# Kernel tuning notes

Hardware: AMD Instinct MI355X
Metric: run time of the kernel (lower is better)

## Reference

```python
import jax, jax.numpy as jnp
from jax import lax
import numpy as np

B, N, E, U = 128, 1024, 300, 128
L = 512          # num_leaves per sample
NN = 2 * L - 1   # num_nodes per sample (binary tree)


def _hsig(x):
    # Keras hard_sigmoid: clip(0.2*x + 0.5, 0, 1)
    return jnp.clip(0.2 * x + 0.5, 0.0, 1.0)


def setup_inputs() -> dict:
    key = jax.random.key(0)
    ks = jax.random.split(key, 5)
    rng = np.random.default_rng(0)
    # children of node t are uniform in [0, t) -> valid bottom-up binary tree
    u = rng.random((B, N, 2))
    child = (u * np.arange(N)[None, :, None]).astype(np.int32)
    child[:, :L, :] = 0  # leaves have no children (never read)
    num_vecs = np.tile(np.array([[NN, L]], np.int32), (B, 1))
    return {
        "initial_state": jax.random.normal(ks[0], (B, N, E), jnp.float32),
        "translation_kernel": jax.random.normal(ks[1], (E, U), jnp.float32) * 0.05,
        "kernel": jax.random.normal(ks[2], (5 * U, U), jnp.float32) * 0.05,
        "recurrent_kernel": jax.random.normal(ks[3], (5 * U, 2 * U), jnp.float32) * 0.05,
        "bias": jnp.zeros((5 * U, 1), jnp.float32),
        "child_vecs": jnp.asarray(child),
        "num_vecs": jnp.asarray(num_vecs),
    }


def reference(initial_state, translation_kernel, kernel, recurrent_kernel, bias,
              child_vecs, num_vecs):
    b, n, _ = initial_state.shape
    units = kernel.shape[1]
    # leaf initial states: relu(x @ W_translate)  -> [B, N, U]
    x = jax.nn.relu(jnp.einsum('bne,eu->bnu', initial_state, translation_kernel))
    num_nodes = num_vecs[:, 0]
    num_leaves = num_vecs[:, 1]
    bvec = bias[:, 0][None, :]  # [1, 5U]

    def step(carry, t):
        H, C = carry  # [B, N, U] each
        ch = jnp.take(child_vecs, t, axis=1)                                   # [B, 2]
        h_ch = jnp.take_along_axis(H, ch[:, :, None], axis=1).reshape(b, 2 * units)
        c_ch = jnp.take_along_axis(C, ch[:, :, None], axis=1).reshape(b, 2 * units)
        xt = jnp.take(x, t, axis=1)                                            # [B, U]
        # z = kernel @ x^T + recurrent_kernel @ [h_l; h_r] + bias  (batched, [B, 5U])
        z = xt @ kernel.T + h_ch @ recurrent_kernel.T + bvec
        i = _hsig(z[:, :units])
        f = _hsig(z[:, units:3 * units])                                       # [B, 2U]
        o = _hsig(z[:, 3 * units:4 * units])
        g = jnp.tanh(z[:, 4 * units:])
        # faithful to original: reshape (flat_mem*f) as [U, 2] row-major, sum axis 1
        c_new = (c_ch * f).reshape(b, units, 2).sum(axis=-1) + i * g
        h_new = o * jnp.tanh(c_new)
        act = ((t >= num_leaves) & (t < num_nodes))[:, None]                   # [B, 1]
        h_upd = jnp.where(act, h_new, jnp.take(H, t, axis=1))
        c_upd = jnp.where(act, c_new, jnp.take(C, t, axis=1))
        H = lax.dynamic_update_slice(H, h_upd[:, None, :], (0, t, 0))
        C = lax.dynamic_update_slice(C, c_upd[:, None, :], (0, t, 0))
        return (H, C), None

    # leaves start with hidden = memory = translated vec; internal nodes overwritten in order
    (H, _), _ = lax.scan(step, (x, x), jnp.arange(n))
    valid = (jnp.arange(n)[None, :] < num_nodes[:, None])[..., None]
    return H * valid.astype(H.dtype)
```

## Files before the change

### kernel.cpp

```cpp
#include <hip/hip_runtime.h>
#include <hip/hip_bf16.h>

#define B_ 128
#define N_ 1024
#define E_ 300
#define U_ 128
#define M_ (B_ * N_)
#define Z_ (5 * U_)
#define LMAXT 40
#define LPAR 14

typedef __attribute__((ext_vector_type(8))) short bf16x8;
typedef __attribute__((ext_vector_type(4))) float f32x4;
typedef _Float16 h2_t __attribute__((ext_vector_type(2)));
typedef _Float16 f16x4 __attribute__((ext_vector_type(4)));
typedef _Float16 f16x8 __attribute__((ext_vector_type(8)));

__device__ __forceinline__ short f2bf(float f) {
  unsigned u = __builtin_bit_cast(unsigned, f);
  u = (u + 0x7fffu + ((u >> 16) & 1u)) >> 16;
  return (short)u;
}

__device__ __forceinline__ float hsig(float z) {
  float v = __builtin_fmaf(z, 0.2f, 0.5f);
  v = v < 0.f ? 0.f : v;
  v = v > 1.f ? 1.f : v;
  return v;
}

__device__ __forceinline__ float tanh_fast(float x) {
  float p = __expf(2.f * x);
  return 1.f - 2.f * __builtin_amdgcn_rcpf(p + 1.f);
}

__device__ __forceinline__ unsigned pk2(float a, float b) {
  return __builtin_bit_cast(unsigned, __builtin_amdgcn_cvt_pkrtz(a, b));
}

__global__ __launch_bounds__(256) void x_gemm(
    const float* __restrict__ A, const float* __restrict__ W,
    float* __restrict__ H, float* __restrict__ C) {
  __shared__ __align__(16) short As[64][40];
  __shared__ __align__(16) short Ws[128][40];
  const int tid = threadIdx.x;
  const int m0 = blockIdx.x * 64;
  f32x4 acc[8] = {};
  const int lane = tid & 63, wv = tid >> 6;
  const int lr = lane & 15, lg = lane >> 4;

  for (int kc = 0; kc < 10; ++kc) {
    const int k0 = kc * 32;
    {
      const int row = tid >> 2, kk = (tid & 3) * 8;
      const float* src = A + (size_t)(m0 + row) * E_ + k0 + kk;
      bf16x8 v;
      if (k0 + 32 <= E_) {
#pragma unroll
        for (int i = 0; i < 8; ++i) v[i] = f2bf(src[i]);
      } else {
#pragma unroll
        for (int i = 0; i < 8; ++i)
          v[i] = (k0 + kk + i < E_) ? f2bf(src[i]) : (short)0;
      }
      *(bf16x8*)&As[row][kk] = v;
    }
#pragma unroll
    for (int s = 0; s < 2; ++s) {
      const int slot = tid + s * 256;
      const int n = slot & 127, kg = slot >> 7;
      bf16x8 v;
      if (k0 + 32 <= E_) {
#pragma unroll
        for (int i = 0; i < 8; ++i) v[i] = f2bf(W[(k0 + kg * 8 + i) * U_ + n]);
      } else {
#pragma unroll
        for (int i = 0; i < 8; ++i) {
          const int k = k0 + kg * 8 + i;
          v[i] = (k < E_) ? f2bf(W[k * U_ + n]) : (short)0;
        }
      }
      *(bf16x8*)&Ws[n][kg * 8] = v;
    }
    __syncthreads();
    bf16x8 a = *(const bf16x8*)&As[wv * 16 + lr][lg * 8];
#pragma unroll
    for (int nt = 0; nt < 8; ++nt) {
      bf16x8 b = *(const bf16x8*)&Ws[nt * 16 + lr][lg * 8];
      acc[nt] = __builtin_amdgcn_mfma_f32_16x16x32_bf16(a, b, acc[nt], 0, 0, 0);
    }
    __syncthreads();
  }
#pragma unroll
  for (int nt = 0; nt < 8; ++nt) {
#pragma unroll
    for (int r = 0; r < 4; ++r) {
      const int m = m0 + wv * 16 + lg * 4 + r;
      const int n = nt * 16 + lr;
      float v = acc[nt][r];
      v = v > 0.f ? v : 0.f;
      H[(size_t)m * U_ + n] = v;
      C[(size_t)m * U_ + n] = v;
    }
  }
}

__global__ __launch_bounds__(256) void xz_gemm(
    const float* __restrict__ X, const float* __restrict__ K,
    const float* __restrict__ bias, const int* __restrict__ nv,
    _Float16* __restrict__ XZ) {
  const int m0 = blockIdx.x * 64;
  {
    const int bb = m0 >> 10;
    const int t0 = m0 & (N_ - 1);
    const int nodes = nv[2 * bb], leaves = nv[2 * bb + 1];
    if (t0 + 64 <= leaves || t0 >= nodes) return;
  }
  __shared__ __align__(16) short As[64][40];
  __shared__ __align__(16) short Ws[128][40];
  const int tid = threadIdx.x;
  const int n0 = blockIdx.y * 128;
  f32x4 acc[8] = {};
  const int lane = tid & 63, wv = tid >> 6;
  const int lr = lane & 15, lg = lane >> 4;

  for (int kc = 0; kc < 4; ++kc) {
    const int k0 = kc * 32;
    {
      const int row = tid >> 2, kk = (tid & 3) * 8;
      const float* src = X + (size_t)(m0 + row) * U_ + k0 + kk;
      bf16x8 v;
#pragma unroll
      for (int i = 0; i < 8; ++i) v[i] = f2bf(src[i]);
      *(bf16x8*)&As[row][kk] = v;
    }
#pragma unroll
    for (int s = 0; s < 2; ++s) {
      const int slot = tid + s * 256;
      const int n = slot >> 2, kk = (slot & 3) * 8;
      const float* src = K + (size_t)(n0 + n) * U_ + k0 + kk;
      bf16x8 v;
#pragma unroll
      for (int i = 0; i < 8; ++i) v[i] = f2bf(src[i]);
      *(bf16x8*)&Ws[n][kk] = v;
    }
    __syncthreads();
    bf16x8 a = *(const bf16x8*)&As[wv * 16 + lr][lg * 8];
#pragma unroll
    for (int nt = 0; nt < 8; ++nt) {
      bf16x8 b = *(const bf16x8*)&Ws[nt * 16 + lr][lg * 8];
      acc[nt] = __builtin_amdgcn_mfma_f32_16x16x32_bf16(a, b, acc[nt], 0, 0, 0);
    }
    __syncthreads();
  }
#pragma unroll
  for (int nt = 0; nt < 8; ++nt) {
    const int n = n0 + nt * 16 + lr;
    const float bv = bias[n];
#pragma unroll
    for (int r = 0; r < 4; ++r) {
      const int m = m0 + wv * 16 + lg * 4 + r;
      XZ[(size_t)m * Z_ + n] = (_Float16)(acc[nt][r] + bv);
    }
  }
}

__global__ __launch_bounds__(256) void wcvt(const float* __restrict__ Wr,
                                            _Float16* __restrict__ W16) {
  const int i = (blockIdx.x * 256 + threadIdx.x) * 2;
  if (i < 640 * 256) {
    W16[i] = (_Float16)Wr[i];
    W16[i + 1] = (_Float16)Wr[i + 1];
  }
}

__global__ __launch_bounds__(512) void levelize(
    const int* __restrict__ child, const int* __restrict__ nv,
    int* __restrict__ lv, int* __restrict__ rank, int* __restrict__ cnt) {
  const int b = blockIdx.x;
  const int tid = threadIdx.x;
  int nodes = nv[2 * b];
  int leaves = nv[2 * b + 1];
  if (nodes > N_) nodes = N_;
  if (leaves < 0) leaves = 0;

  __shared__ short lvs[N_];
  __shared__ int chs[2 * N_];
  __shared__ int cnts[LMAXT];
  __shared__ int changed;

  for (int i = tid; i < N_; i += 512) lvs[i] = 0;
  for (int i = tid; i < 2 * N_; i += 512) chs[i] = child[(size_t)b * 2 * N_ + i];
  if (tid < LMAXT) cnts[tid] = 0;
  __syncthreads();

  int stable = 0;
  for (int s = 0; s < 64; ++s) {
    if (tid == 0) changed = 0;
    __syncthreads();
    int any = 0;
    for (int t = leaves + tid; t < nodes; t += 512) {
      const int c0 = chs[2 * t], c1 = chs[2 * t + 1];
      const int l0 = (c0 < t && c0 >= 0) ? lvs[c0] : 0;
      const int l1 = (c1 < t && c1 >= 0) ? lvs[c1] : 0;
      const int l = 1 + (l0 > l1 ? l0 : l1);
      if (l > (int)lvs[t]) { lvs[t] = (short)l; any = 1; }
    }
    if (any) changed = 1;
    __syncthreads();
    if (!changed) { stable = 1; break; }
  }
  if (!stable) {
    if (tid == 0) {
      for (int t = leaves; t < nodes; ++t) {
        const int c0 = chs[2 * t], c1 = chs[2 * t + 1];
        const int l0 = (c0 < t && c0 >= 0) ? lvs[c0] : 0;
        const int l1 = (c1 < t && c1 >= 0) ? lvs[c1] : 0;
        lvs[t] = (short)(1 + (l0 > l1 ? l0 : l1));
      }
    }
    __syncthreads();
  }

  for (int t = leaves + tid; t < nodes; t += 512) {
    int l = lvs[t];
    if (l > LMAXT - 1) l = LMAXT - 1;
    lv[b * N_ + t] = l;
    if (l < LMAXT - 1) rank[b * N_ + t] = atomicAdd(&cnts[l], 1);
  }
  __syncthreads();
  if (tid == 0) {
    for (int t = leaves; t < nodes; ++t)
      if ((int)lvs[t] >= LMAXT - 1) rank[b * N_ + t] = cnts[LMAXT - 1]++;
  }
  __syncthreads();
  if (tid < LMAXT) cnt[tid * 128 + b] = cnts[tid];
}

__global__ __launch_bounds__(64) void offsets(
    const int* __restrict__ cnt, int* __restrict__ pos, int* __restrict__ goff) {
  const int l = threadIdx.x;
  __shared__ int tot[LMAXT];
  if (l < LMAXT) {
    int s = 0;
    for (int b = 0; b < 128; ++b) {
      pos[l * 128 + b] = s;
      s += cnt[l * 128 + b];
    }
    tot[l] = s;
  }
  __syncthreads();
  if (l == 0) {
    int g = 0;
    for (int i = 0; i < LMAXT; ++i) { goff[i] = g; g += tot[i]; }
    goff[LMAXT] = g;
  }
  __syncthreads();
  if (l < LMAXT) {
    const int g = goff[l];
    for (int b = 0; b < 128; ++b) pos[l * 128 + b] += g;
  }
}

__global__ __launch_bounds__(256) void scatter_zero(
    const int* __restrict__ nv, const int* __restrict__ lv,
    const int* __restrict__ rank, const int* __restrict__ pos,
    int* __restrict__ glist, float* __restrict__ H) {
  const int b = blockIdx.x;
  const int tid = threadIdx.x;
  int nodes = nv[2 * b];
  int leaves = nv[2 * b + 1];
  if (nodes > N_) nodes = N_;
  if (leaves < 0) leaves = 0;
  for (int t = leaves + tid; t < nodes; t += 256) {
    const int l = lv[b * N_ + t];
    glist[pos[l * 128 + b] + rank[b * N_ + t]] = (b << 10) | t;
  }
  const int total = (N_ - nodes) * U_;
  for (int idx = tid; idx < total; idx += 256)
    H[(size_t)b * N_ * U_ + nodes * U_ + idx] = 0.f;
}

__global__ __launch_bounds__(512, 2) void level_gemm(
    int lvl, const _Float16* __restrict__ W16, const int* __restrict__ child,
    const int* __restrict__ goff, const int* __restrict__ glist,
    const _Float16* __restrict__ XZ, float* __restrict__ H,
    float* __restrict__ C) {
  const int base = goff[lvl];
  const int count = goff[lvl + 1] - base;
  if (count <= 0) return;
  const int tid = threadIdx.x;
  const int lane = tid & 63, w = tid >> 6;
  const int col = lane & 15, hi = lane >> 4;
  const int u0 = 16 * w + 4 * hi;
  const int mc = 2 * u0;

  f16x8 afrag[5][8];
  {
    const int rows[5] = {16 * w + col, 128 + 32 * w + 2 * col,
                         129 + 32 * w + 2 * col, 384 + 16 * w + col,
                         512 + 16 * w + col};
#pragma unroll
    for (int rt = 0; rt < 5; ++rt) {
      const _Float16* rs = W16 + (size_t)rows[rt] * 256 + 8 * hi;
#pragma unroll
      for (int kt = 0; kt < 8; ++kt) afrag[rt][kt] = *(const f16x8*)(rs + 32 * kt);
    }
  }

  __shared__ __align__(16) _Float16 hbuf[16][272];

  const int nchunk = (count + 15) >> 4;
  for (int chunk = blockIdx.x; chunk < nchunk; chunk += gridDim.x) {
    const int cb = base + chunk * 16;
    int rem = count - chunk * 16;
    if (rem > 16) rem = 16;

    const int j = tid >> 5, s = tid & 31;
    const int nidj = glist[cb + (j < rem ? j : rem - 1)];
    const int bj = nidj >> 10, tj = nidj & 1023;
    const int chj = child[((size_t)bj << 11) + 2 * tj + (s >> 4)];
    const float* hsrc =
        H + (((size_t)(bj << 10) + chj) << 7) + ((s & 15) << 3);
    const float4 a0 = *(const float4*)hsrc;
    const float4 a1 = *(const float4*)(hsrc + 4);

    const int nidc = glist[cb + (col < rem ? col : rem - 1)];
    const int bc = nidc >> 10, tc = nidc & 1023;
    const _Float16* xzr = XZ + ((size_t)((bc << 10) | tc)) * Z_;
    const f16x4 xzi = *(const f16x4*)(xzr + u0);
    const f16x8 xzf = *(const f16x8*)(xzr + 128 + mc);
    const f16x4 xzo = *(const f16x4*)(xzr + 384 + u0);
    const f16x4 xzg = *(const f16x4*)(xzr + 512 + u0);
    const int csel = child[((size_t)bc << 11) + 2 * tc + (mc >> 7)];
    const float* cbp = C + (((size_t)(bc << 10) + csel) << 7) + (mc & 127);
    const float4 cv0 = ((const float4*)cbp)[0];
    const float4 cv1 = ((const float4*)cbp)[1];

    uint4 hp;
    hp.x = pk2(a0.x, a0.y);
    hp.y = pk2(a0.z, a0.w);
    hp.z = pk2(a1.x, a1.y);
    hp.w = pk2(a1.z, a1.w);
    *(uint4*)&hbuf[j][(s >> 4) * 128 + (s & 15) * 8] = hp;
    __syncthreads();

    f32x4 acc[5];
#pragma unroll
    for (int r = 0; r < 4; ++r) {
      acc[0][r] = (float)xzi[r];
      acc[1][r] = (float)xzf[2 * r];
      acc[2][r] = (float)xzf[2 * r + 1];
      acc[3][r] = (float)xzo[r];
      acc[4][r] = (float)xzg[r];
    }
#pragma unroll
    for (int kt = 0; kt < 8; ++kt) {
      const f16x8 bf = *(const f16x8*)&hbuf[col][32 * kt + 8 * hi];
#pragma unroll
      for (int rt = 0; rt < 5; ++rt)
        acc[rt] = __builtin_amdgcn_mfma_f32_16x16x32_f16(afrag[rt][kt], bf,
                                                         acc[rt], 0, 0, 0);
    }

    const float ce[8] = {cv0.x, cv0.y, cv0.z, cv0.w,
                         cv1.x, cv1.y, cv1.z, cv1.w};
    f32x4 hn4, cn4;
#pragma unroll
    for (int r = 0; r < 4; ++r) {
      const float cn = ce[2 * r] * hsig(acc[1][r]) +
                       ce[2 * r + 1] * hsig(acc[2][r]) +
                       hsig(acc[0][r]) * tanh_fast(acc[4][r]);
      cn4[r] = cn;
      hn4[r] = hsig(acc[3][r]) * tanh_fast(cn);
    }
    if (col < rem) {
      const size_t rowb = ((size_t)((bc << 10) | tc)) << 7;
      *(f32x4*)(H + rowb + u0) = hn4;
      *(f32x4*)(C + rowb + u0) = cn4;
    }
    __syncthreads();
  }
}

__global__ __launch_bounds__(512, 2) void tail_scan(
    const _Float16* __restrict__ W16, const int* __restrict__ child,
    const int* __restrict__ nv, const int* __restrict__ pos,
    const int* __restrict__ cnt, const int* __restrict__ glist,
    const _Float16* __restrict__ XZ, float* __restrict__ H,
    float* __restrict__ C) {
  const int b = blockIdx.x;
  const int tid = threadIdx.x;
  const int lane = tid & 63, w = tid >> 6;
  const int col = lane & 15, hi = lane >> 4;
  const int u0 = 16 * w + 4 * hi;
  const int mc = 2 * u0;
  const int m4 = 4 * lane;

  f16x8 afrag[5][8];
  {
    const int rows[5] = {16 * w + col, 128 + 32 * w + 2 * col,
                         129 + 32 * w + 2 * col, 384 + 16 * w + col,
                         512 + 16 * w + col};
#pragma unroll
    for (int rt = 0; rt < 5; ++rt) {
      const _Float16* rs = W16 + (size_t)rows[rt] * 256 + 8 * hi;
#pragma unroll
      for (int kt = 0; kt < 8; ++kt) afrag[rt][kt] = *(const f16x8*)(rs + 32 * kt);
    }
  }

  __shared__ __align__(16) _Float16 hb1[256];
  const int* chb = child + (size_t)b * 2 * N_;
  float* Hb = H + (size_t)b * N_ * U_;
  float* Cb = C + (size_t)b * N_ * U_;
  const _Float16* xzb = XZ + (size_t)b * N_ * Z_;

  for (int l = LPAR; l < LMAXT; ++l) {
    const int p0 = pos[l * 128 + b];
    const int n = cnt[l * 128 + b];
    for (int i = 0; i < n; ++i) {
      const int t = glist[p0 + i] & 1023;
      if (tid < 64) {
        const int ch = chb[2 * t + (m4 >> 7)];
        const float4 hv = *(const float4*)(Hb + ((size_t)ch << 7) + (m4 & 127));
        uint2 hp;
        hp.x = pk2(hv.x, hv.y);
        hp.y = pk2(hv.z, hv.w);
        *(uint2*)&hb1[m4] = hp;
      }
      const int cs = chb[2 * t + (mc >> 7)];
      const float* cbp = Cb + ((size_t)cs << 7) + (mc & 127);
      const float4 cv0 = ((const float4*)cbp)[0];
      const float4 cv1 = ((const float4*)cbp)[1];
      const _Float16* xzr = xzb + (size_t)t * Z_;
      const f16x4 xzi = *(const f16x4*)(xzr + u0);
      const f16x8 xzf = *(const f16x8*)(xzr + 128 + mc);
      const f16x4 xzo = *(const f16x4*)(xzr + 384 + u0);
      const f16x4 xzg = *(const f16x4*)(xzr + 512 + u0);
      __syncthreads();
      f32x4 acc[5];
#pragma unroll
      for (int r = 0; r < 4; ++r) {
        acc[0][r] = (float)xzi[r];
        acc[1][r] = (float)xzf[2 * r];
        acc[2][r] = (float)xzf[2 * r + 1];
        acc[3][r] = (float)xzo[r];
        acc[4][r] = (float)xzg[r];
      }
#pragma unroll
      for (int kt = 0; kt < 8; ++kt) {
        const f16x8 bf = *(const f16x8*)&hb1[32 * kt + 8 * hi];
#pragma unroll
        for (int rt = 0; rt < 5; ++rt)
          acc[rt] = __builtin_amdgcn_mfma_f32_16x16x32_f16(afrag[rt][kt], bf,
                                                           acc[rt], 0, 0, 0);
      }
      const float ce[8] = {cv0.x, cv0.y, cv0.z, cv0.w,
                           cv1.x, cv1.y, cv1.z, cv1.w};
      f32x4 hn4, cn4;
#pragma unroll
      for (int r = 0; r < 4; ++r) {
        const float cn = ce[2 * r] * hsig(acc[1][r]) +
                         ce[2 * r + 1] * hsig(acc[2][r]) +
                         hsig(acc[0][r]) * tanh_fast(acc[4][r]);
        cn4[r] = cn;
        hn4[r] = hsig(acc[3][r]) * tanh_fast(cn);
      }
      if (col == 0) {
        *(f32x4*)(Hb + ((size_t)t << 7) + u0) = hn4;
        *(f32x4*)(Cb + ((size_t)t << 7) + u0) = cn4;
      }
      __syncthreads();
    }
  }
}

__global__ __launch_bounds__(512, 2) void tree_scan6(
    const float* __restrict__ Wr, const int* __restrict__ child,
    const int* __restrict__ nv, const _Float16* __restrict__ XZ,
    float* __restrict__ H, float* __restrict__ Cst) {
  const int b = blockIdx.x;
  const int tid = threadIdx.x;
  const int lane = tid & 63, w = tid >> 6;
  const int col = lane & 15, hi = lane >> 4;
  int nodes = nv[2 * b];
  int leaves = nv[2 * b + 1];
  if (nodes > N_) nodes = N_;
  if (leaves < 0) leaves = 0;
  float* Hb = H + (size_t)b * N_ * U_;
  float* Cb = Cst + (size_t)b * N_ * U_;
  const int* chb = child + (size_t)b * N_ * 2;
  const _Float16* xzb = XZ + (size_t)b * N_ * Z_;

  f16x8 afrag[5][8];
  {
    const int rows[5] = {16 * w + col, 128 + 32 * w + 2 * col,
                         129 + 32 * w + 2 * col, 384 + 16 * w + col,
                         512 + 16 * w + col};
#pragma unroll
    for (int rt = 0; rt < 5; ++rt) {
      const float* rs = Wr + (size_t)rows[rt] * 256 + 8 * hi;
#pragma unroll
      for (int kt = 0; kt < 8; ++kt) {
#pragma unroll
        for (int i = 0; i < 8; ++i)
          afrag[rt][kt][i] = (_Float16)rs[32 * kt + i];
      }
    }
  }

  __shared__ __align__(16) _Float16 hbuf[8][256];
  const int u0 = 16 * w + 4 * hi;
  const int mc = 2 * u0;
  const int m4 = 4 * lane;

  if (leaves < nodes) {
    int2 ccT = *(const int2*)(chb + 2 * leaves);
    float4 hv = *(const float4*)(Hb + (size_t)(lane < 32 ? ccT.x : ccT.y) * U_ +
                                 (m4 & 127));
    const float* cbp = Cb + (size_t)(w < 4 ? ccT.x : ccT.y) * U_ + (mc & 127);
    float4 cv0 = ((const float4*)cbp)[0];
    float4 cv1 = ((const float4*)cbp)[1];
    f16x4 xzi = *(const f16x4*)(xzb + (size_t)leaves * Z_ + u0);
    f16x8 xzf = *(const f16x8*)(xzb + (size_t)leaves * Z_ + 128 + mc);
    f16x4 xzo = *(const f16x4*)(xzb + (size_t)leaves * Z_ + 384 + u0);
    f16x4 xzg = *(const f16x4*)(xzb + (size_t)leaves * Z_ + 512 + u0);
    const int tn1 = (leaves + 1 < nodes) ? leaves + 1 : leaves;
    int2 ccN = *(const int2*)(chb + 2 * tn1);

    for (int t = leaves; t < nodes; ++t) {
      const int tn = (t + 1 < nodes) ? t + 1 : t;
      if (t > leaves) {
        if (ccT.x == t - 1 && lane < 32)
          hv = *(const float4*)(Hb + (size_t)(t - 1) * U_ + m4);
        if (ccT.y == t - 1 && lane >= 32)
          hv = *(const float4*)(Hb + (size_t)(t - 1) * U_ + (m4 & 127));
        const int crow = (w < 4) ? ccT.x : ccT.y;
        if (crow == t - 1) {
          const float* cpp = Cb + (size_t)(t - 1) * U_ + (mc & 127);
          cv0 = ((const float4*)cpp)[0];
          cv1 = ((const float4*)cpp)[1];
        }
      }
      uint2 hp;
      hp.x = pk2(hv.x, hv.y);
      hp.y = pk2(hv.z, hv.w);
      *(uint2*)&hbuf[w][m4] = hp;
      __builtin_amdgcn_sched_barrier(0);
      float4 hv_n = *(const float4*)(
          Hb + (size_t)(lane < 32 ? ccN.x : ccN.y) * U_ + (m4 & 127));
      const float* cbn = Cb + (size_t)(w < 4 ? ccN.x : ccN.y) * U_ + (mc & 127);
      const float4 cv0n = ((const float4*)cbn)[0];
      const float4 cv1n = ((const float4*)cbn)[1];
      const f16x4 xzi_n = *(const f16x4*)(xzb + (size_t)tn * Z_ + u0);
      const f16x8 xzf_n = *(const f16x8*)(xzb + (size_t)tn * Z_ + 128 + mc);
      const f16x4 xzo_n = *(const f16x4*)(xzb + (size_t)tn * Z_ + 384 + u0);
      const f16x4 xzg_n = *(const f16x4*)(xzb + (size_t)tn * Z_ + 512 + u0);
      const int tnn = (t + 2 < nodes) ? t + 2 : nodes - 1;
      const int2 ccNN = *(const int2*)(chb + 2 * tnn);
      __builtin_amdgcn_sched_barrier(0);
      f16x8 bfrag[8];
#pragma unroll
      for (int kt = 0; kt < 8; ++kt)
        bfrag[kt] = *(const f16x8*)&hbuf[w][32 * kt + 8 * hi];
      f32x4 acc[5] = {};
#pragma unroll
      for (int kt = 0; kt < 8; ++kt) {
#pragma unroll
        for (int rt = 0; rt < 5; ++rt)
          acc[rt] = __builtin_amdgcn_mfma_f32_16x16x32_f16(
              afrag[rt][kt], bfrag[kt], acc[rt], 0, 0, 0);
      }
      const float ce[8] = {cv0.x, cv0.y, cv0.z, cv0.w,
                           cv1.x, cv1.y, cv1.z, cv1.w};
      f32x4 hn4, cn4;
#pragma unroll
      for (int r = 0; r < 4; ++r) {
        const float zi = acc[0][r] + (float)xzi[r];
        const float zf0 = acc[1][r] + (float)xzf[2 * r];
        const float zf1 = acc[2][r] + (float)xzf[2 * r + 1];
        const float zo = acc[3][r] + (float)xzo[r];
        const float zg = acc[4][r] + (float)xzg[r];
        const float cn = ce[2 * r] * hsig(zf0) + ce[2 * r + 1] * hsig(zf1) +
                         hsig(zi) * tanh_fast(zg);
        cn4[r] = cn;
        hn4[r] = hsig(zo) * tanh_fast(cn);
      }
      if (col == 0) {
        *(f32x4*)(Hb + (size_t)t * U_ + u0) = hn4;
        *(f32x4*)(Cb + (size_t)t * U_ + u0) = cn4;
      }
      asm volatile("s_waitcnt lgkmcnt(0)" ::: "memory");
      __builtin_amdgcn_sched_barrier(0);
      __builtin_amdgcn_s_barrier();
      __builtin_amdgcn_sched_barrier(0);
      hv = hv_n; cv0 = cv0n; cv1 = cv1n;
      xzi = xzi_n; xzf = xzf_n; xzo = xzo_n; xzg = xzg_n;
      ccT = ccN; ccN = ccNN;
    }
  }
  const int total = (N_ - nodes) * U_;
  for (int idx = tid; idx < total; idx += 512)
    Hb[(size_t)nodes * U_ + idx] = 0.f;
}

extern "C" void kernel_launch(void* const* d_in, const int* in_sizes, int n_in,
                              void* d_out, int out_size, void* d_ws,
                              size_t ws_size, hipStream_t stream) {
  const float* state = (const float*)d_in[0];
  const float* tk    = (const float*)d_in[1];
  const float* Wk    = (const float*)d_in[2];
  const float* Wr    = (const float*)d_in[3];
  const float* bias  = (const float*)d_in[4];
  const int*   child = (const int*)d_in[5];
  const int*   nvp   = (const int*)d_in[6];
  float* H = (float*)d_out;

  const size_t MB = 1024ull * 1024ull;
  const size_t meta_sz = 2 * MB;
  const size_t c_bytes = (size_t)M_ * U_ * sizeof(float);
  const size_t xz_bytes = (size_t)M_ * Z_ * sizeof(_Float16);

  if (ws_size >= meta_sz + c_bytes + xz_bytes) {
    char* wsb = (char*)d_ws;
    _Float16* W16 = (_Float16*)(wsb + 0x0);
    int* lv    = (int*)(wsb + 0x50000);
    int* rank  = (int*)(wsb + 0xD0000);
    int* cnt   = (int*)(wsb + 0x150000);
    int* pos   = (int*)(wsb + 0x158000);
    int* goff  = (int*)(wsb + 0x160000);
    int* glist = (int*)(wsb + 0x161000);
    float* C = (float*)(wsb + meta_sz);
    _Float16* XZ = (_Float16*)(wsb + meta_sz + c_bytes);

    x_gemm<<<M_ / 64, 256, 0, stream>>>(state, tk, H, C);
    wcvt<<<320, 256, 0, stream>>>(Wr, W16);
    xz_gemm<<<dim3(M_ / 64, 5), 256, 0, stream>>>(H, Wk, bias, nvp, XZ);
    levelize<<<B_, 512, 0, stream>>>(child, nvp, lv, rank, cnt);
    offsets<<<1, 64, 0, stream>>>(cnt, pos, goff);
    scatter_zero<<<B_, 256, 0, stream>>>(nvp, lv, rank, pos, glist, H);
    static const int lg[LPAR] = {0, 512, 512, 256, 256, 128, 128,
                                 64, 64, 64, 32, 32, 32, 32};
    for (int l = 1; l < LPAR; ++l)
      level_gemm<<<lg[l], 512, 0, stream>>>(l, W16, child, goff, glist, XZ, H,
                                            C);
    tail_scan<<<B_, 512, 0, stream>>>(W16, child, nvp, pos, cnt, glist, XZ, H,
                                      C);
  } else {
    float* C = (float*)d_ws;
    _Float16* XZ = (_Float16*)((char*)d_ws + c_bytes);
    x_gemm<<<M_ / 64, 256, 0, stream>>>(state, tk, H, C);
    xz_gemm<<<dim3(M_ / 64, 5), 256, 0, stream>>>(H, Wk, bias, nvp, XZ);
    tree_scan6<<<B_, 512, 0, stream>>>(Wr, child, nvp, XZ, H, C);
  }
}
```

Before: 413.3 us.

## Fuse translation and input-projection GEMMs, pre-convert weights, extend level-parallel phase

Merges the leaf translation GEMM and the input-gate projection GEMM into one kernel. The relu'd translated rows stay in shared memory as fp16 and are reused for the XZ projection, so H is not re-read from global memory. A single prep kernel pre-converts the recurrent kernel, the input kernel and the transposed translation kernel to fp16. This removes the per-block bf16 conversion and shared-memory weight staging. The number of levels handled by the batched level GEMM rises from 14 to 20, shrinking the sequential tail scan. Level and rank metadata shrink to byte and short widths, and the small-workspace fallback is removed. The changes trade bf16 for fp16 in the translation GEMM, and each block now does the whole 640-wide projection serially.

```diff
diff --git a/kernel.cpp b/kernel.cpp
--- a/kernel.cpp
+++ b/kernel.cpp
@@ -8,19 +8,11 @@
 #define M_ (B_ * N_)
 #define Z_ (5 * U_)
 #define LMAXT 40
-#define LPAR 14
-
-typedef __attribute__((ext_vector_type(8))) short bf16x8;
+#define LPAR 20
+
 typedef __attribute__((ext_vector_type(4))) float f32x4;
-typedef _Float16 h2_t __attribute__((ext_vector_type(2)));
 typedef _Float16 f16x4 __attribute__((ext_vector_type(4)));
 typedef _Float16 f16x8 __attribute__((ext_vector_type(8)));
-
-__device__ __forceinline__ short f2bf(float f) {
-  unsigned u = __builtin_bit_cast(unsigned, f);
-  u = (u + 0x7fffu + ((u >> 16) & 1u)) >> 16;
-  return (short)u;
-}
 
 __device__ __forceinline__ float hsig(float z) {
   float v = __builtin_fmaf(z, 0.2f, 0.5f);
@@ -38,145 +30,128 @@
   return __builtin_bit_cast(unsigned, __builtin_amdgcn_cvt_pkrtz(a, b));
 }
 
-__global__ __launch_bounds__(256) void x_gemm(
-    const float* __restrict__ A, const float* __restrict__ W,
-    float* __restrict__ H, float* __restrict__ C) {
-  __shared__ __align__(16) short As[64][40];
-  __shared__ __align__(16) short Ws[128][40];
+__device__ __forceinline__ f16x8 pack8(float4 a, float4 b) {
+  uint4 u;
+  u.x = pk2(a.x, a.y);
+  u.y = pk2(a.z, a.w);
+  u.z = pk2(b.x, b.y);
+  u.w = pk2(b.z, b.w);
+  return __builtin_bit_cast(f16x8, u);
+}
+
+__global__ __launch_bounds__(256) void prep(
+    const float* __restrict__ Wr, const float* __restrict__ Wk,
+    const float* __restrict__ tk, _Float16* __restrict__ W16,
+    _Float16* __restrict__ Wk16, _Float16* __restrict__ tkT16) {
+  const int idx = blockIdx.x * 256 + threadIdx.x;
+  if (idx < 163840) {
+    W16[idx] = (_Float16)Wr[idx];
+  } else if (idx < 245760) {
+    const int i = idx - 163840;
+    Wk16[i] = (_Float16)Wk[i];
+  } else if (idx < 286720) {
+    const int i = idx - 245760;
+    const int n = i / 320, k = i - n * 320;
+    tkT16[i] = (k < E_) ? (_Float16)tk[k * U_ + n] : (_Float16)0.f;
+  }
+}
+
+__global__ __launch_bounds__(256) void fused_gemm(
+    const float* __restrict__ state, const _Float16* __restrict__ tkT16,
+    const _Float16* __restrict__ Wk16, const float* __restrict__ bias,
+    const int* __restrict__ nv, float* __restrict__ H, float* __restrict__ C,
+    _Float16* __restrict__ XZ) {
   const int tid = threadIdx.x;
+  const int lane = tid & 63, wv = tid >> 6;
+  const int lr = lane & 15, hi = lane >> 4;
   const int m0 = blockIdx.x * 64;
+  const int bb = m0 >> 10, t0 = m0 & (N_ - 1);
+  const int nodes = nv[2 * bb], leaves = nv[2 * bb + 1];
+  const bool active = (t0 + 64 > leaves) && (t0 < nodes);
+
+  __shared__ __align__(16) _Float16 xls[64][136];
+
   f32x4 acc[8] = {};
-  const int lane = tid & 63, wv = tid >> 6;
-  const int lr = lane & 15, lg = lane >> 4;
-
+  const float* arow = state + (size_t)(m0 + wv * 16 + lr) * E_;
+#pragma unroll
   for (int kc = 0; kc < 10; ++kc) {
     const int k0 = kc * 32;
-    {
-      const int row = tid >> 2, kk = (tid & 3) * 8;
-      const float* src = A + (size_t)(m0 + row) * E_ + k0 + kk;
-      bf16x8 v;
-      if (k0 + 32 <= E_) {
-#pragma unroll
-        for (int i = 0; i < 8; ++i) v[i] = f2bf(src[i]);
-      } else {
-#pragma unroll
-        for (int i = 0; i < 8; ++i)
-          v[i] = (k0 + kk + i < E_) ? f2bf(src[i]) : (short)0;
-      }
-      *(bf16x8*)&As[row][kk] = v;
-    }
-#pragma unroll
-    for (int s = 0; s < 2; ++s) {
-      const int slot = tid + s * 256;
-      const int n = slot & 127, kg = slot >> 7;
-      bf16x8 v;
-      if (k0 + 32 <= E_) {
-#pragma unroll
-        for (int i = 0; i < 8; ++i) v[i] = f2bf(W[(k0 + kg * 8 + i) * U_ + n]);
-      } else {
-#pragma unroll
-        for (int i = 0; i < 8; ++i) {
-          const int k = k0 + kg * 8 + i;
-          v[i] = (k < E_) ? f2bf(W[k * U_ + n]) : (short)0;
-        }
-      }
-      *(bf16x8*)&Ws[n][kg * 8] = v;
-    }
-    __syncthreads();
-    bf16x8 a = *(const bf16x8*)&As[wv * 16 + lr][lg * 8];
+    f16x8 af;
+    if (kc < 9) {
+      const float4 a0 = *(const float4*)(arow + k0 + 8 * hi);
+      const float4 a1 = *(const float4*)(arow + k0 + 8 * hi + 4);
+      af = pack8(a0, a1);
+    } else {
+      float4 a0 = {0.f, 0.f, 0.f, 0.f}, a1 = {0.f, 0.f, 0.f, 0.f};
+      if (hi == 0) {
+        a0 = *(const float4*)(arow + 288);
+        a1 = *(const float4*)(arow + 292);
+      } else if (hi == 1) {
+        a0 = *(const float4*)(arow + 296);
+      }
+      af = pack8(a0, a1);
+    }
 #pragma unroll
     for (int nt = 0; nt < 8; ++nt) {
-      bf16x8 b = *(const bf16x8*)&Ws[nt * 16 + lr][lg * 8];
-      acc[nt] = __builtin_amdgcn_mfma_f32_16x16x32_bf16(a, b, acc[nt], 0, 0, 0);
-    }
-    __syncthreads();
-  }
+      const f16x8 bf =
+          *(const f16x8*)(tkT16 + (size_t)(nt * 16 + lr) * 320 + k0 + 8 * hi);
+      acc[nt] = __builtin_amdgcn_mfma_f32_16x16x32_f16(af, bf, acc[nt], 0, 0, 0);
+    }
+  }
+
 #pragma unroll
   for (int nt = 0; nt < 8; ++nt) {
 #pragma unroll
     for (int r = 0; r < 4; ++r) {
-      const int m = m0 + wv * 16 + lg * 4 + r;
-      const int n = nt * 16 + lr;
       float v = acc[nt][r];
       v = v > 0.f ? v : 0.f;
-      H[(size_t)m * U_ + n] = v;
-      C[(size_t)m * U_ + n] = v;
-    }
-  }
-}
-
-__global__ __launch_bounds__(256) void xz_gemm(
-    const float* __restrict__ X, const float* __restrict__ K,
-    const float* __restrict__ bias, const int* __restrict__ nv,
-    _Float16* __restrict__ XZ) {
-  const int m0 = blockIdx.x * 64;
+      xls[wv * 16 + hi * 4 + r][nt * 16 + lr] = (_Float16)v;
+    }
+  }
+  __syncthreads();
+
   {
-    const int bb = m0 >> 10;
-    const int t0 = m0 & (N_ - 1);
-    const int nodes = nv[2 * bb], leaves = nv[2 * bb + 1];
-    if (t0 + 64 <= leaves || t0 >= nodes) return;
-  }
-  __shared__ __align__(16) short As[64][40];
-  __shared__ __align__(16) short Ws[128][40];
-  const int tid = threadIdx.x;
-  const int n0 = blockIdx.y * 128;
-  f32x4 acc[8] = {};
-  const int lane = tid & 63, wv = tid >> 6;
-  const int lr = lane & 15, lg = lane >> 4;
-
-  for (int kc = 0; kc < 4; ++kc) {
-    const int k0 = kc * 32;
-    {
-      const int row = tid >> 2, kk = (tid & 3) * 8;
-      const float* src = X + (size_t)(m0 + row) * U_ + k0 + kk;
-      bf16x8 v;
-#pragma unroll
-      for (int i = 0; i < 8; ++i) v[i] = f2bf(src[i]);
-      *(bf16x8*)&As[row][kk] = v;
-    }
-#pragma unroll
-    for (int s = 0; s < 2; ++s) {
-      const int slot = tid + s * 256;
-      const int n = slot >> 2, kk = (slot & 3) * 8;
-      const float* src = K + (size_t)(n0 + n) * U_ + k0 + kk;
-      bf16x8 v;
-#pragma unroll
-      for (int i = 0; i < 8; ++i) v[i] = f2bf(src[i]);
-      *(bf16x8*)&Ws[n][kk] = v;
-    }
-    __syncthreads();
-    bf16x8 a = *(const bf16x8*)&As[wv * 16 + lr][lg * 8];
-#pragma unroll
-    for (int nt = 0; nt < 8; ++nt) {
-      bf16x8 b = *(const bf16x8*)&Ws[nt * 16 + lr][lg * 8];
-      acc[nt] = __builtin_amdgcn_mfma_f32_16x16x32_bf16(a, b, acc[nt], 0, 0, 0);
-    }
-    __syncthreads();
-  }
-#pragma unroll
-  for (int nt = 0; nt < 8; ++nt) {
-    const int n = n0 + nt * 16 + lr;
-    const float bv = bias[n];
-#pragma unroll
-    for (int r = 0; r < 4; ++r) {
-      const int m = m0 + wv * 16 + lg * 4 + r;
-      XZ[(size_t)m * Z_ + n] = (_Float16)(acc[nt][r] + bv);
-    }
-  }
-}
-
-__global__ __launch_bounds__(256) void wcvt(const float* __restrict__ Wr,
-                                            _Float16* __restrict__ W16) {
-  const int i = (blockIdx.x * 256 + threadIdx.x) * 2;
-  if (i < 640 * 256) {
-    W16[i] = (_Float16)Wr[i];
-    W16[i + 1] = (_Float16)Wr[i + 1];
+    const int row = tid >> 2, c0 = (tid & 3) * 32;
+    const size_t base = (size_t)(m0 + row) * U_;
+#pragma unroll
+    for (int s = 0; s < 4; ++s) {
+      const f16x8 v = *(const f16x8*)&xls[row][c0 + 8 * s];
+      const float4 lo = {(float)v[0], (float)v[1], (float)v[2], (float)v[3]};
+      const float4 hi4 = {(float)v[4], (float)v[5], (float)v[6], (float)v[7]};
+      *(float4*)(H + base + c0 + 8 * s) = lo;
+      *(float4*)(H + base + c0 + 8 * s + 4) = hi4;
+      *(float4*)(C + base + c0 + 8 * s) = lo;
+      *(float4*)(C + base + c0 + 8 * s + 4) = hi4;
+    }
+  }
+
+  if (active) {
+    f16x8 pa[4];
+#pragma unroll
+    for (int kk = 0; kk < 4; ++kk)
+      pa[kk] = *(const f16x8*)&xls[wv * 16 + lr][kk * 32 + 8 * hi];
+#pragma unroll 4
+    for (int nt = 0; nt < 40; ++nt) {
+      const int n = nt * 16 + lr;
+      const float bv = bias[n];
+      f32x4 a2 = {bv, bv, bv, bv};
+#pragma unroll
+      for (int kk = 0; kk < 4; ++kk) {
+        const f16x8 bf =
+            *(const f16x8*)(Wk16 + (size_t)n * U_ + kk * 32 + 8 * hi);
+        a2 = __builtin_amdgcn_mfma_f32_16x16x32_f16(pa[kk], bf, a2, 0, 0, 0);
+      }
+#pragma unroll
+      for (int r = 0; r < 4; ++r)
+        XZ[(size_t)(m0 + wv * 16 + hi * 4 + r) * Z_ + n] = (_Float16)a2[r];
+    }
   }
 }
 
 __global__ __launch_bounds__(512) void levelize(
     const int* __restrict__ child, const int* __restrict__ nv,
-    int* __restrict__ lv, int* __restrict__ rank, int* __restrict__ cnt) {
+    unsigned char* __restrict__ lv, short* __restrict__ rank,
+    int* __restrict__ cnt) {
   const int b = blockIdx.x;
   const int tid = threadIdx.x;
   int nodes = nv[2 * b];
@@ -225,13 +200,13 @@
   for (int t = leaves + tid; t < nodes; t += 512) {
     int l = lvs[t];
     if (l > LMAXT - 1) l = LMAXT - 1;
-    lv[b * N_ + t] = l;
-    if (l < LMAXT - 1) rank[b * N_ + t] = atomicAdd(&cnts[l], 1);
+    lv[b * N_ + t] = (unsigned char)l;
+    if (l < LMAXT - 1) rank[b * N_ + t] = (short)atomicAdd(&cnts[l], 1);
   }
   __syncthreads();
   if (tid == 0) {
     for (int t = leaves; t < nodes; ++t)
-      if ((int)lvs[t] >= LMAXT - 1) rank[b * N_ + t] = cnts[LMAXT - 1]++;
+      if ((int)lvs[t] >= LMAXT - 1) rank[b * N_ + t] = (short)(cnts[LMAXT - 1]++);
   }
   __syncthreads();
   if (tid < LMAXT) cnt[tid * 128 + b] = cnts[tid];
@@ -263,8 +238,8 @@
 }
 
 __global__ __launch_bounds__(256) void scatter_zero(
-    const int* __restrict__ nv, const int* __restrict__ lv,
-    const int* __restrict__ rank, const int* __restrict__ pos,
+    const int* __restrict__ nv, const unsigned char* __restrict__ lv,
+    const short* __restrict__ rank, const int* __restrict__ pos,
     int* __restrict__ glist, float* __restrict__ H) {
   const int b = blockIdx.x;
   const int tid = threadIdx.x;
@@ -320,8 +295,7 @@
     const int nidj = glist[cb + (j < rem ? j : rem - 1)];
     const int bj = nidj >> 10, tj = nidj & 1023;
     const int chj = child[((size_t)bj << 11) + 2 * tj + (s >> 4)];
-    const float* hsrc =
-        H + (((size_t)(bj << 10) + chj) << 7) + ((s & 15) << 3);
+    const float* hsrc = H + (((size_t)(bj << 10) + chj) << 7) + ((s & 15) << 3);
     const float4 a0 = *(const float4*)hsrc;
     const float4 a1 = *(const float4*)(hsrc + 4);
 
@@ -476,135 +450,6 @@
   }
 }
 
-__global__ __launch_bounds__(512, 2) void tree_scan6(
-    const float* __restrict__ Wr, const int* __restrict__ child,
-    const int* __restrict__ nv, const _Float16* __restrict__ XZ,
-    float* __restrict__ H, float* __restrict__ Cst) {
-  const int b = blockIdx.x;
-  const int tid = threadIdx.x;
-  const int lane = tid & 63, w = tid >> 6;
-  const int col = lane & 15, hi = lane >> 4;
-  int nodes = nv[2 * b];
-  int leaves = nv[2 * b + 1];
-  if (nodes > N_) nodes = N_;
-  if (leaves < 0) leaves = 0;
-  float* Hb = H + (size_t)b * N_ * U_;
-  float* Cb = Cst + (size_t)b * N_ * U_;
-  const int* chb = child + (size_t)b * N_ * 2;
-  const _Float16* xzb = XZ + (size_t)b * N_ * Z_;
-
-  f16x8 afrag[5][8];
-  {
-    const int rows[5] = {16 * w + col, 128 + 32 * w + 2 * col,
-                         129 + 32 * w + 2 * col, 384 + 16 * w + col,
-                         512 + 16 * w + col};
-#pragma unroll
-    for (int rt = 0; rt < 5; ++rt) {
-      const float* rs = Wr + (size_t)rows[rt] * 256 + 8 * hi;
-#pragma unroll
-      for (int kt = 0; kt < 8; ++kt) {
-#pragma unroll
-        for (int i = 0; i < 8; ++i)
-          afrag[rt][kt][i] = (_Float16)rs[32 * kt + i];
-      }
-    }
-  }
-
-  __shared__ __align__(16) _Float16 hbuf[8][256];
-  const int u0 = 16 * w + 4 * hi;
-  const int mc = 2 * u0;
-  const int m4 = 4 * lane;
-
-  if (leaves < nodes) {
-    int2 ccT = *(const int2*)(chb + 2 * leaves);
-    float4 hv = *(const float4*)(Hb + (size_t)(lane < 32 ? ccT.x : ccT.y) * U_ +
-                                 (m4 & 127));
-    const float* cbp = Cb + (size_t)(w < 4 ? ccT.x : ccT.y) * U_ + (mc & 127);
-    float4 cv0 = ((const float4*)cbp)[0];
-    float4 cv1 = ((const float4*)cbp)[1];
-    f16x4 xzi = *(const f16x4*)(xzb + (size_t)leaves * Z_ + u0);
-    f16x8 xzf = *(const f16x8*)(xzb + (size_t)leaves * Z_ + 128 + mc);
-    f16x4 xzo = *(const f16x4*)(xzb + (size_t)leaves * Z_ + 384 + u0);
-    f16x4 xzg = *(const f16x4*)(xzb + (size_t)leaves * Z_ + 512 + u0);
-    const int tn1 = (leaves + 1 < nodes) ? leaves + 1 : leaves;
-    int2 ccN = *(const int2*)(chb + 2 * tn1);
-
-    for (int t = leaves; t < nodes; ++t) {
-      const int tn = (t + 1 < nodes) ? t + 1 : t;
-      if (t > leaves) {
-        if (ccT.x == t - 1 && lane < 32)
-          hv = *(const float4*)(Hb + (size_t)(t - 1) * U_ + m4);
-        if (ccT.y == t - 1 && lane >= 32)
-          hv = *(const float4*)(Hb + (size_t)(t - 1) * U_ + (m4 & 127));
-        const int crow = (w < 4) ? ccT.x : ccT.y;
-        if (crow == t - 1) {
-          const float* cpp = Cb + (size_t)(t - 1) * U_ + (mc & 127);
-          cv0 = ((const float4*)cpp)[0];
-          cv1 = ((const float4*)cpp)[1];
-        }
-      }
-      uint2 hp;
-      hp.x = pk2(hv.x, hv.y);
-      hp.y = pk2(hv.z, hv.w);
-      *(uint2*)&hbuf[w][m4] = hp;
-      __builtin_amdgcn_sched_barrier(0);
-      float4 hv_n = *(const float4*)(
-          Hb + (size_t)(lane < 32 ? ccN.x : ccN.y) * U_ + (m4 & 127));
-      const float* cbn = Cb + (size_t)(w < 4 ? ccN.x : ccN.y) * U_ + (mc & 127);
-      const float4 cv0n = ((const float4*)cbn)[0];
-      const float4 cv1n = ((const float4*)cbn)[1];
-      const f16x4 xzi_n = *(const f16x4*)(xzb + (size_t)tn * Z_ + u0);
-      const f16x8 xzf_n = *(const f16x8*)(xzb + (size_t)tn * Z_ + 128 + mc);
-      const f16x4 xzo_n = *(const f16x4*)(xzb + (size_t)tn * Z_ + 384 + u0);
-      const f16x4 xzg_n = *(const f16x4*)(xzb + (size_t)tn * Z_ + 512 + u0);
-      const int tnn = (t + 2 < nodes) ? t + 2 : nodes - 1;
-      const int2 ccNN = *(const int2*)(chb + 2 * tnn);
-      __builtin_amdgcn_sched_barrier(0);
-      f16x8 bfrag[8];
-#pragma unroll
-      for (int kt = 0; kt < 8; ++kt)
-        bfrag[kt] = *(const f16x8*)&hbuf[w][32 * kt + 8 * hi];
-      f32x4 acc[5] = {};
-#pragma unroll
-      for (int kt = 0; kt < 8; ++kt) {
-#pragma unroll
-        for (int rt = 0; rt < 5; ++rt)
-          acc[rt] = __builtin_amdgcn_mfma_f32_16x16x32_f16(
-              afrag[rt][kt], bfrag[kt], acc[rt], 0, 0, 0);
-      }
-      const float ce[8] = {cv0.x, cv0.y, cv0.z, cv0.w,
-                           cv1.x, cv1.y, cv1.z, cv1.w};
-      f32x4 hn4, cn4;
-#pragma unroll
-      for (int r = 0; r < 4; ++r) {
-        const float zi = acc[0][r] + (float)xzi[r];
-        const float zf0 = acc[1][r] + (float)xzf[2 * r];
-        const float zf1 = acc[2][r] + (float)xzf[2 * r + 1];
-        const float zo = acc[3][r] + (float)xzo[r];
-        const float zg = acc[4][r] + (float)xzg[r];
-        const float cn = ce[2 * r] * hsig(zf0) + ce[2 * r + 1] * hsig(zf1) +
-                         hsig(zi) * tanh_fast(zg);
-        cn4[r] = cn;
-        hn4[r] = hsig(zo) * tanh_fast(cn);
-      }
-      if (col == 0) {
-        *(f32x4*)(Hb + (size_t)t * U_ + u0) = hn4;
-        *(f32x4*)(Cb + (size_t)t * U_ + u0) = cn4;
-      }
-      asm volatile("s_waitcnt lgkmcnt(0)" ::: "memory");
-      __builtin_amdgcn_sched_barrier(0);
-      __builtin_amdgcn_s_barrier();
-      __builtin_amdgcn_sched_barrier(0);
-      hv = hv_n; cv0 = cv0n; cv1 = cv1n;
-      xzi = xzi_n; xzf = xzf_n; xzo = xzo_n; xzg = xzg_n;
-      ccT = ccN; ccN = ccNN;
-    }
-  }
-  const int total = (N_ - nodes) * U_;
-  for (int idx = tid; idx < total; idx += 512)
-    Hb[(size_t)nodes * U_ + idx] = 0.f;
-}
-
 extern "C" void kernel_launch(void* const* d_in, const int* in_sizes, int n_in,
                               void* d_out, int out_size, void* d_ws,
                               size_t ws_size, hipStream_t stream) {
@@ -617,41 +462,30 @@
   const int*   nvp   = (const int*)d_in[6];
   float* H = (float*)d_out;
 
-  const size_t MB = 1024ull * 1024ull;
-  const size_t meta_sz = 2 * MB;
+  char* wsb = (char*)d_ws;
+  _Float16* W16   = (_Float16*)(wsb + 0x000000);
+  _Float16* Wk16  = (_Float16*)(wsb + 0x050000);
+  _Float16* tkT16 = (_Float16*)(wsb + 0x078000);
+  unsigned char* lv = (unsigned char*)(wsb + 0x08C000);
+  short* rank     = (short*)(wsb + 0x0AC000);
+  int* cnt        = (int*)(wsb + 0x0EC000);
+  int* pos        = (int*)(wsb + 0x0F1000);
+  int* goff       = (int*)(wsb + 0x0F6000);
+  int* glist      = (int*)(wsb + 0x0F7000);
+  const size_t meta_sz = 2ull * 1024 * 1024;
   const size_t c_bytes = (size_t)M_ * U_ * sizeof(float);
-  const size_t xz_bytes = (size_t)M_ * Z_ * sizeof(_Float16);
-
-  if (ws_size >= meta_sz + c_bytes + xz_bytes) {
-    char* wsb = (char*)d_ws;
-    _Float16* W16 = (_Float16*)(wsb + 0x0);
-    int* lv    = (int*)(wsb + 0x50000);
-    int* rank  = (int*)(wsb + 0xD0000);
-    int* cnt   = (int*)(wsb + 0x150000);
-    int* pos   = (int*)(wsb + 0x158000);
-    int* goff  = (int*)(wsb + 0x160000);
-    int* glist = (int*)(wsb + 0x161000);
-    float* C = (float*)(wsb + meta_sz);
-    _Float16* XZ = (_Float16*)(wsb + meta_sz + c_bytes);
-
-    x_gemm<<<M_ / 64, 256, 0, stream>>>(state, tk, H, C);
-    wcvt<<<320, 256, 0, stream>>>(Wr, W16);
-    xz_gemm<<<dim3(M_ / 64, 5), 256, 0, stream>>>(H, Wk, bias, nvp, XZ);
-    levelize<<<B_, 512, 0, stream>>>(child, nvp, lv, rank, cnt);
-    offsets<<<1, 64, 0, stream>>>(cnt, pos, goff);
-    scatter_zero<<<B_, 256, 0, stream>>>(nvp, lv, rank, pos, glist, H);
-    static const int lg[LPAR] = {0, 512, 512, 256, 256, 128, 128,
-                                 64, 64, 64, 32, 32, 32, 32};
-    for (int l = 1; l < LPAR; ++l)
-      level_gemm<<<lg[l], 512, 0, stream>>>(l, W16, child, goff, glist, XZ, H,
-                                            C);
-    tail_scan<<<B_, 512, 0, stream>>>(W16, child, nvp, pos, cnt, glist, XZ, H,
-                                      C);
-  } else {
-    float* C = (float*)d_ws;
-    _Float16* XZ = (_Float16*)((char*)d_ws + c_bytes);
-    x_gemm<<<M_ / 64, 256, 0, stream>>>(state, tk, H, C);
-    xz_gemm<<<dim3(M_ / 64, 5), 256, 0, stream>>>(H, Wk, bias, nvp, XZ);
-    tree_scan6<<<B_, 512, 0, stream>>>(Wr, child, nvp, XZ, H, C);
-  }
-}
+  float* C = (float*)(wsb + meta_sz);
+  _Float16* XZ = (_Float16*)(wsb + meta_sz + c_bytes);
+
+  prep<<<1120, 256, 0, stream>>>(Wr, Wk, tk, W16, Wk16, tkT16);
+  fused_gemm<<<M_ / 64, 256, 0, stream>>>(state, tkT16, Wk16, bias, nvp, H, C,
+                                          XZ);
+  levelize<<<B_, 512, 0, stream>>>(child, nvp, lv, rank, cnt);
+  offsets<<<1, 64, 0, stream>>>(cnt, pos, goff);
+  scatter_zero<<<B_, 256, 0, stream>>>(nvp, lv, rank, pos, glist, H);
+  static const int lg[LPAR] = {0,  512, 512, 256, 256, 128, 128, 64, 64, 64,
+                               32, 32,  32,  32,  32,  32,  16,  16, 16, 16};
+  for (int l = 1; l < LPAR; ++l)
+    level_gemm<<<lg[l], 512, 0, stream>>>(l, W16, child, goff, glist, XZ, H, C);
+  tail_scan<<<B_, 512, 0, stream>>>(W16, child, nvp, pos, cnt, glist, XZ, H, C);
+}
```

After: 541.2 us. +30.9%, slower.
